# Kernel tuning notes

Hardware: AMD Instinct MI355X
Metric: run time of the kernel (lower is better)

Reference implementation:

```python
import jax, jax.numpy as jnp
import numpy as np

B, DIM, H, W = 32, 512, 48, 24


def conv1x1(x, w, b):
    # x: [B,C,H,W], w: [O,C], b: [O]  (torch Conv2d 1x1 weight squeezed)
    return jnp.einsum('bchw,oc->bohw', x, w) + b[None, :, None, None]


def setup_inputs() -> dict:
    key = jax.random.key(0)
    ks = jax.random.split(key, 14)
    s = 0.02
    inp = {
        'x': jax.random.normal(ks[0], (B, DIM, H, W), jnp.float32),
        'x_h': jax.random.normal(ks[1], (B, DIM, H, W), jnp.float32),
        'Wg': jax.random.normal(ks[2], (DIM, DIM), jnp.float32) * s,
        'bg': jax.random.normal(ks[3], (DIM,), jnp.float32) * s,
        'Wt': jax.random.normal(ks[4], (DIM, DIM), jnp.float32) * s,
        'bt': jax.random.normal(ks[5], (DIM,), jnp.float32) * s,
        'Wp': jax.random.normal(ks[6], (DIM, DIM), jnp.float32) * s,
        'bp': jax.random.normal(ks[7], (DIM,), jnp.float32) * s,
        'Ww': jax.random.normal(ks[8], (DIM, DIM), jnp.float32) * s,
        'bw': jax.random.normal(ks[9], (DIM,), jnp.float32) * s,
        'gamma': jax.random.normal(ks[10], (DIM,), jnp.float32) * 0.1,
        'beta': jax.random.normal(ks[11], (DIM,), jnp.float32) * 0.1,
        'run_mean': jax.random.normal(ks[12], (DIM,), jnp.float32) * 0.1,
        'run_var': jax.random.uniform(ks[13], (DIM,), jnp.float32, 0.5, 1.5),
    }
    return inp


def reference(x, x_h, Wg, bg, Wt, bt, Wp, bp, Ww, bw, gamma, beta, run_mean, run_var):
    Bsz, dim = x.shape[0], Wg.shape[0]
    g_x = conv1x1(x_h, Wg, bg).reshape(Bsz, dim, -1)      # [B,dim,N]
    theta_x = conv1x1(x, Wt, bt).reshape(Bsz, dim, -1)    # [B,dim,N]
    phi_x = conv1x1(x_h, Wp, bp).reshape(Bsz, dim, -1)    # [B,dim,N]
    # energy[b,i,j] = sum_n theta[b,i,n] * phi[b,j,n]  -> channel attention [B,dim,dim]
    energy = jnp.einsum('bin,bjn->bij', theta_x, phi_x)
    attention = energy / dim  # energy.size(-1) == dim
    y = jnp.einsum('bij,bjn->bin', attention, g_x).reshape(Bsz, dim, *x_h.shape[2:])
    W_y = conv1x1(y, Ww, bw)
    # BatchNorm2d in eval mode
    inv = gamma / jnp.sqrt(run_var + 1e-5)
    W_y = (W_y - run_mean[None, :, None, None]) * inv[None, :, None, None] + beta[None, :, None, None]
    return W_y + x
```

## Files before the change

kernel.cpp:

```cpp
#include <hip/hip_runtime.h>
#include <stdint.h>

typedef short short8 __attribute__((ext_vector_type(8)));
typedef float f32x4 __attribute__((ext_vector_type(4)));
typedef unsigned short u16;
typedef unsigned int u32;

struct alignas(8) U16x4 { u16 x, y, z, w; };

__device__ __forceinline__ u16 f2bf(float f) {
  u32 u = __float_as_uint(f);
  u += 0x7fffu + ((u >> 16) & 1u);
  return (u16)(u >> 16);
}
__device__ __forceinline__ float bf2f(u16 v) {
  return __uint_as_float(((u32)v) << 16);
}

__device__ __forceinline__ void gld_lds16(const u16* g, u16* l) {
  __builtin_amdgcn_global_load_lds((const __attribute__((address_space(1))) u32*)g,
                                   (__attribute__((address_space(3))) u32*)l,
                                   16, 0, 0);
}

__device__ __forceinline__ void mfma16x16x32(f32x4& c, short8 a, short8 b) {
  asm("v_mfma_f32_16x16x32_bf16 %0, %1, %2, %0" : "+v"(c) : "v"(a), "v"(b));
}

__device__ __forceinline__ float wave_red(float v) {
  for (int off = 32; off; off >>= 1) v += __shfl_down(v, off);
  return v;
}

template<int EPI>
__global__ void __launch_bounds__(512, 2) gemm_abt(
                         const u16* __restrict__ A, int64_t Abs,
                         const u16* __restrict__ Bt, int64_t Bbs,
                         void* __restrict__ Cptr, int64_t Cbs,
                         int M, int N, int K,
                         const float* __restrict__ v1,
                         const float* __restrict__ v2,
                         const float* __restrict__ v3,
                         const float* __restrict__ v4,
                         const u16* __restrict__ xres) {
  constexpr int BM = 256, BN = 128, BK = 32;
  extern __shared__ u16 lds[];
  u16* ldsA = lds;
  u16* ldsB = lds + 4 * (BM * BK);

  int bx, by, b;
  if (gridDim.z == 1) {
    const int nbx = N >> 7;
    const int bpb = nbx * (M >> 8);
    const int id = blockIdx.x;
    const int xcd = id & 7, rest = id >> 3;
    b = xcd + 8 * (rest / bpb);
    const int wi = rest % bpb;
    by = wi / nbx; bx = wi % nbx;
  } else {
    bx = blockIdx.x; by = blockIdx.y; b = blockIdx.z;
  }

  const u16* Ab = A + (int64_t)b * Abs;
  const u16* Bb = Bt + (int64_t)b * Bbs;
  const int brow = by * BM, bcol = bx * BN;
  const int tid = threadIdx.x, lane = tid & 63, w = tid >> 6;
  const int wr = w >> 1, wc = w & 1;

  f32x4 acc[4][4] = {};

  const int sr = tid >> 2;
  const int scs = ((tid & 3) ^ (sr & 3)) * 8;
  const int lo = sr * BK + (tid & 3) * 8;
  const u16* gA = Ab + (int64_t)(brow + sr) * K + scs;
  const u16* gB = Bb + (int64_t)(bcol + sr) * K + scs;

  const int la16 = lane & 15;
  const int kg = (lane >> 4) * 8;
  const int kc = kg ^ ((la16 & 3) * 8);
  const int nt = K / BK;

#define STAGE(buf, k0)                                              \
  do {                                                              \
    u16* la_ = ldsA + (buf) * (BM * BK) + lo;                       \
    u16* lb_ = ldsB + (buf) * (BN * BK) + lo;                       \
    gld_lds16(gA + (k0), la_);                                      \
    gld_lds16(gA + (int64_t)128 * K + (k0), la_ + 128 * BK);        \
    gld_lds16(gB + (k0), lb_);                                      \
  } while (0)

  STAGE(0, 0);
  STAGE(1, BK);
  STAGE(2, 2 * BK);

  for (int t = 0; t < nt; ++t) {
    __builtin_amdgcn_s_barrier();
    if (t + 3 < nt) {
      STAGE((t + 3) & 3, (t + 3) * BK);
      asm volatile("s_waitcnt vmcnt(9)" ::: "memory");
    } else {
      const int rem = nt - 1 - t;
      if (rem == 2)      asm volatile("s_waitcnt vmcnt(6)" ::: "memory");
      else if (rem == 1) asm volatile("s_waitcnt vmcnt(3)" ::: "memory");
      else               asm volatile("s_waitcnt vmcnt(0)" ::: "memory");
    }
    __builtin_amdgcn_s_barrier();
    __builtin_amdgcn_sched_barrier(0);
    const u16* as = ldsA + (t & 3) * (BM * BK);
    const u16* bs = ldsB + (t & 3) * (BN * BK);
    short8 af[4], bf[4];
#pragma unroll
    for (int m = 0; m < 4; ++m)
      af[m] = *(const short8*)&as[(wr * 64 + m * 16 + la16) * BK + kc];
#pragma unroll
    for (int n = 0; n < 4; ++n)
      bf[n] = *(const short8*)&bs[(wc * 64 + n * 16 + la16) * BK + kc];
    __builtin_amdgcn_s_setprio(1);
#pragma unroll
    for (int m = 0; m < 4; ++m)
#pragma unroll
      for (int n = 0; n < 4; ++n)
        mfma16x16x32(acc[m][n], af[m], bf[n]);
    __builtin_amdgcn_s_setprio(0);
  }
#undef STAGE
  asm volatile("s_nop 7\n\ts_nop 7");

  const int r0 = brow + wr * 64 + (lane >> 4) * 4;
  const int c0 = bcol + wc * 64 + la16;
  const int64_t b512 = (int64_t)b * 512;

  if (EPI == 4) {
    float* Cb = (float*)Cptr + (int64_t)b * Cbs;
    const u16* xb = xres + (int64_t)b * Cbs;
#pragma unroll
    for (int m = 0; m < 4; ++m) {
#pragma unroll
      for (int r = 0; r < 4; ++r) {
        const int row = r0 + m * 16 + r;
        const float scl = v1[row], shf = v2[b512 + row];
#pragma unroll
        for (int n = 0; n < 4; ++n) {
          const int col = c0 + n * 16;
          Cb[(int64_t)row * N + col] =
              acc[m][n][r] * scl + shf + bf2f(xb[(int64_t)row * N + col]);
        }
      }
    }
  } else {
    u16* Cb = (u16*)Cptr + (int64_t)b * Cbs;
#pragma unroll
    for (int m = 0; m < 4; ++m) {
#pragma unroll
      for (int r = 0; r < 4; ++r) {
        const int row = r0 + m * 16 + r;
        float a1 = 0.f, a3 = 0.f;
        if (EPI == 6) { a1 = v1[b512 + row]; a3 = v3[row]; }
#pragma unroll
        for (int n = 0; n < 4; ++n) {
          const int col = c0 + n * 16;
          float v = acc[m][n][r];
          if (EPI == 6) v += a1 * v2[col] + a3 * v4[b512 + col];
          Cb[(int64_t)row * N + col] = f2bf(v);
        }
      }
    }
  }
}

__global__ void prep_all(const float* __restrict__ x, const float* __restrict__ xh,
                         u16* __restrict__ xB, u16* __restrict__ xhB,
                         u16* __restrict__ xhT,
                         float* __restrict__ rx_part, float* __restrict__ rxh_part) {
  __shared__ float tl[64][65];
  __shared__ float rs[64];
  const int z = blockIdx.z;
  const int b = z & 31;
  const bool isxh = z >= 32;
  const float* src = (isxh ? xh : x) + (int64_t)b * 589824;
  u16* dstB = (isxh ? xhB : xB) + (int64_t)b * 589824;
  const int n0 = blockIdx.x * 64, c0 = blockIdx.y * 64;
  const int t = threadIdx.x;
  const int cl = t >> 4;
  const int q = t & 15;
#pragma unroll
  for (int p = 0; p < 4; ++p) {
    const int row = p * 16 + cl;
    const float4 v = *(const float4*)&src[(int64_t)(c0 + row) * 1152 + n0 + q * 4];
    tl[row][q * 4] = v.x; tl[row][q * 4 + 1] = v.y;
    tl[row][q * 4 + 2] = v.z; tl[row][q * 4 + 3] = v.w;
    U16x4 o = {f2bf(v.x), f2bf(v.y), f2bf(v.z), f2bf(v.w)};
    *(U16x4*)&dstB[(int64_t)(c0 + row) * 1152 + n0 + q * 4] = o;
    float pr = v.x + v.y + v.z + v.w;
    pr += __shfl_down(pr, 8); pr += __shfl_down(pr, 4);
    pr += __shfl_down(pr, 2); pr += __shfl_down(pr, 1);
    if (q == 0) rs[row] = pr;
  }
  __syncthreads();
  if (t < 64) {
    float* part = isxh ? rxh_part : rx_part;
    part[blockIdx.x * 16384 + b * 512 + c0 + t] = rs[t];
  }
  if (isxh) {
    const int n = t >> 2, cb = (t & 3) * 16;
    u16* dT = xhT + (int64_t)b * 589824 + (int64_t)(n0 + n) * 512 + c0 + cb;
#pragma unroll
    for (int j = 0; j < 4; ++j) {
      U16x4 o = {f2bf(tl[cb + 4 * j][n]), f2bf(tl[cb + 4 * j + 1][n]),
                 f2bf(tl[cb + 4 * j + 2][n]), f2bf(tl[cb + 4 * j + 3][n])};
      *(U16x4*)&dT[4 * j] = o;
    }
  }
}

__global__ void transpose_cvt4(const float* __restrict__ s0, const float* __restrict__ s1,
                               const float* __restrict__ s2, const float* __restrict__ s3,
                               u16* __restrict__ d0, u16* __restrict__ d1,
                               u16* __restrict__ d2, u16* __restrict__ d3) {
  const int z = blockIdx.z;
  const float* in = z == 0 ? s0 : z == 1 ? s1 : z == 2 ? s2 : s3;
  u16* out = z == 0 ? d0 : z == 1 ? d1 : z == 2 ? d2 : d3;
  __shared__ float t[32][33];
  const int n0 = blockIdx.x * 32, c0 = blockIdx.y * 32;
  const int tr = threadIdx.x >> 3, tc = (threadIdx.x & 7) * 4;
  const float4 v = *(const float4*)&in[(int64_t)(c0 + tr) * 512 + n0 + tc];
  t[tr][tc] = v.x; t[tr][tc + 1] = v.y; t[tr][tc + 2] = v.z; t[tr][tc + 3] = v.w;
  __syncthreads();
  U16x4 o;
  o.x = f2bf(t[tc][tr]); o.y = f2bf(t[tc + 1][tr]);
  o.z = f2bf(t[tc + 2][tr]); o.w = f2bf(t[tc + 3][tr]);
  *(U16x4*)&out[(int64_t)(n0 + tr) * 512 + c0 + tc] = o;
}

__global__ void cvt_kernel(const float* __restrict__ in, u16* __restrict__ out, int n4) {
  const int i = blockIdx.x * 256 + threadIdx.x;
  if (i < n4) {
    const float4 v = ((const float4*)in)[i];
    U16x4 o = {f2bf(v.x), f2bf(v.y), f2bf(v.z), f2bf(v.w)};
    ((U16x4*)out)[i] = o;
  }
}

__global__ void k_misc(const float* __restrict__ rx_part, const float* __restrict__ rxh_part,
                       float* __restrict__ rx, float* __restrict__ rxh,
                       const float* __restrict__ gamma, const float* __restrict__ beta,
                       const float* __restrict__ mean, const float* __restrict__ var,
                       const float* __restrict__ bw,
                       const float* __restrict__ bp, const float* __restrict__ bg,
                       float* __restrict__ sc2, float* __restrict__ shift0,
                       float* __restrict__ s2) {
  if (blockIdx.x < 64) {
    const int i = blockIdx.x * 256 + threadIdx.x;
    float s = 0;
#pragma unroll 3
    for (int p = 0; p < 18; ++p) s += rxh_part[p * 16384 + i];
    rxh[i] = s;
  } else if (blockIdx.x < 128) {
    const int i = (blockIdx.x - 64) * 256 + threadIdx.x;
    float s = 0;
#pragma unroll 3
    for (int p = 0; p < 18; ++p) s += rx_part[p * 16384 + i];
    rx[i] = s;
  } else {
    for (int c = threadIdx.x; c < 512; c += 256) {
      const float sc = gamma[c] * rsqrtf(var[c] + 1e-5f);
      sc2[c] = sc * (1.0f / 512.0f);
      shift0[c] = (bw[c] - mean[c]) * sc + beta[c];
    }
    if (threadIdx.x < 64) {
      float p = 0;
      for (int k = threadIdx.x; k < 512; k += 64) p += bp[k] * bg[k];
      p = wave_red(p);
      if (threadIdx.x == 0) s2[0] = p;
    }
  }
}

__global__ void k_mv1(const float* __restrict__ Wp, const float* __restrict__ Wt,
                      const float* __restrict__ Ww,
                      const u16* __restrict__ WpT, const u16* __restrict__ WgT,
                      const float* __restrict__ bg, const float* __restrict__ bt,
                      const float* __restrict__ bp,
                      const float* __restrict__ rx, const float* __restrict__ rxh,
                      float* __restrict__ sigphi, float* __restrict__ tau2,
                      float* __restrict__ h1, float* __restrict__ w1,
                      float* __restrict__ c2) {
  const int wid = blockIdx.x * 4 + (threadIdx.x >> 6);
  const int lane = threadIdx.x & 63;
  float dot = 0;
  if (wid < 16384) {
    const int b = wid >> 9, t = wid & 511;
    const float* wr = Wp + (int64_t)t * 512;
    const float* vr = rxh + b * 512;
#pragma unroll
    for (int k = 0; k < 8; ++k) dot += wr[lane + k * 64] * vr[lane + k * 64];
    dot = wave_red(dot);
    if (lane == 0) sigphi[wid] = dot;
  } else if (wid < 32768) {
    const int r = wid - 16384, b = r >> 9, t = r & 511;
    const float* wr = Wt + (int64_t)t * 512;
    const float* vr = rx + b * 512;
#pragma unroll
    for (int k = 0; k < 8; ++k) dot += wr[lane + k * 64] * vr[lane + k * 64];
    dot = wave_red(dot);
    if (lane == 0) tau2[r] = dot + 1152.0f * bt[t];
  } else if (wid < 33280) {
    const int j = wid - 32768;
    const u16* wr = WpT + (int64_t)j * 512;
#pragma unroll
    for (int k = 0; k < 8; ++k) dot += bf2f(wr[lane + k * 64]) * bg[lane + k * 64];
    dot = wave_red(dot);
    if (lane == 0) h1[j] = dot;
  } else if (wid < 33792) {
    const int c = wid - 33280;
    const float* wr = Ww + (int64_t)c * 512;
#pragma unroll
    for (int k = 0; k < 8; ++k) dot += wr[lane + k * 64] * bt[lane + k * 64];
    dot = wave_red(dot);
    if (lane == 0) w1[c] = dot;
  } else {
    const int e = wid - 33792;
    const u16* wr = WgT + (int64_t)e * 512;
#pragma unroll
    for (int k = 0; k < 8; ++k) dot += bf2f(wr[lane + k * 64]) * bp[lane + k * 64];
    dot = wave_red(dot);
    if (lane == 0) c2[e] = dot;
  }
}

__global__ void k_mv2(const u16* __restrict__ WgT, const float* __restrict__ Ww,
                      const float* __restrict__ bg,
                      const float* __restrict__ sigphi, const float* __restrict__ tau2,
                      float* __restrict__ c1, float* __restrict__ w2,
                      float* __restrict__ s1) {
  const int wid = blockIdx.x * 4 + (threadIdx.x >> 6);
  const int lane = threadIdx.x & 63;
  float dot = 0;
  if (wid < 16384) {
    const int b = wid >> 9, t = wid & 511;
    const u16* wr = WgT + (int64_t)t * 512;
    const float* vr = sigphi + b * 512;
#pragma unroll
    for (int k = 0; k < 8; ++k) dot += bf2f(wr[lane + k * 64]) * vr[lane + k * 64];
    dot = wave_red(dot);
    if (lane == 0) c1[wid] = dot;
  } else if (wid < 32768) {
    const int r = wid - 16384, b = r >> 9, t = r & 511;
    const float* wr = Ww + (int64_t)t * 512;
    const float* vr = tau2 + b * 512;
#pragma unroll
    for (int k = 0; k < 8; ++k) dot += wr[lane + k * 64] * vr[lane + k * 64];
    dot = wave_red(dot);
    if (lane == 0) w2[r] = dot;
  } else if (wid < 32800) {
    const int b = wid - 32768;
    const float* vr = sigphi + b * 512;
#pragma unroll
    for (int k = 0; k < 8; ++k) dot += vr[lane + k * 64] * bg[lane + k * 64];
    dot = wave_red(dot);
    if (lane == 0) s1[b] = dot;
  }
}

__global__ void k_shiftv(const u16* __restrict__ R, const float* __restrict__ h1,
                         const float* __restrict__ w1, const float* __restrict__ w2,
                         const float* __restrict__ s1, const float* __restrict__ s2,
                         const float* __restrict__ sc2, const float* __restrict__ shift0,
                         float* __restrict__ shiftv) {
  const int wid = blockIdx.x * 4 + (threadIdx.x >> 6);
  const int lane = threadIdx.x & 63;
  const int b = wid >> 9, c = wid & 511;
  const u16* rr = R + (int64_t)b * 262144 + (int64_t)c * 512;
  float dot = 0;
#pragma unroll
  for (int k = 0; k < 8; ++k) dot += bf2f(rr[lane + k * 64]) * h1[lane + k * 64];
  dot = wave_red(dot);
  if (lane == 0)
    shiftv[wid] = sc2[c] * (dot + s1[b] * w1[c] + s2[0] * w2[wid]) + shift0[c];
}

extern "C" void kernel_launch(void* const* d_in, const int* in_sizes, int n_in,
                              void* d_out, int out_size, void* d_ws, size_t ws_size,
                              hipStream_t stream) {
  const float* x     = (const float*)d_in[0];
  const float* x_h   = (const float*)d_in[1];
  const float* Wg    = (const float*)d_in[2];
  const float* bg    = (const float*)d_in[3];
  const float* Wt    = (const float*)d_in[4];
  const float* bt    = (const float*)d_in[5];
  const float* Wp    = (const float*)d_in[6];
  const float* bp    = (const float*)d_in[7];
  const float* Ww    = (const float*)d_in[8];
  const float* bw    = (const float*)d_in[9];
  const float* gamma = (const float*)d_in[10];
  const float* beta  = (const float*)d_in[11];
  const float* rmean = (const float*)d_in[12];
  const float* rvar  = (const float*)d_in[13];
  float* out = (float*)d_out;

  const int Bsz = 32, D = 512, N = 1152;
  const int64_t DN = (int64_t)D * N;
  const int64_t DD = (int64_t)D * D;
  const size_t LDSB = 98304;

  char* ws = (char*)d_ws;
  const size_t KB = 1024, MB = 1048576;
  u16* WtT  = (u16*)(ws + 0);
  u16* WpT  = (u16*)(ws + 512 * KB);
  u16* WwB  = (u16*)(ws + 1 * MB);
  u16* WgT  = (u16*)(ws + 1 * MB + 512 * KB);
  u16* WaB  = (u16*)(ws + 2 * MB);
  u16* WbTB = (u16*)(ws + 2 * MB + 512 * KB);
  float* rx     = (float*)(ws + 3 * MB + 512 * KB);
  float* rxh    = (float*)(ws + 3 * MB + 576 * KB);
  float* sigphi = (float*)(ws + 3 * MB + 640 * KB);
  float* tau2   = (float*)(ws + 3 * MB + 704 * KB);
  float* c1     = (float*)(ws + 3 * MB + 768 * KB);
  float* w2     = (float*)(ws + 3 * MB + 832 * KB);
  float* shiftv = (float*)(ws + 3 * MB + 896 * KB);
  float* h1     = (float*)(ws + 3 * MB + 960 * KB);
  float* w1     = (float*)(ws + 3 * MB + 962 * KB);
  float* c2     = (float*)(ws + 3 * MB + 964 * KB);
  float* sc2    = (float*)(ws + 3 * MB + 968 * KB);
  float* shift0 = (float*)(ws + 3 * MB + 970 * KB);
  float* s1     = (float*)(ws + 3 * MB + 972 * KB);
  float* s2     = (float*)(ws + 3 * MB + 974 * KB);
  u16* xB  = (u16*)(ws + 4 * MB);
  u16* xhB = (u16*)(ws + 40 * MB);
  u16* xhT = (u16*)(ws + 76 * MB);
  u16* SD1 = (u16*)(ws + 112 * MB);
  u16* SD2 = (u16*)(ws + 130 * MB);
  float* rx_part  = (float*)(ws + 148 * MB);
  float* rxh_part = (float*)(ws + 150 * MB);

  prep_all<<<dim3(18, 8, 64), 256, 0, stream>>>(x, x_h, xB, xhB, xhT,
                                                rx_part, rxh_part);
  transpose_cvt4<<<dim3(16, 16, 4), 256, 0, stream>>>(Wt, Wp, Wg, Ww, WtT, WpT, WgT,
                                                      (u16*)(ws + 152 * MB) );
  cvt_kernel<<<dim3(D * D / 4 / 256), 256, 0, stream>>>(Ww, WwB, D * D / 4);
  k_misc<<<dim3(129), 256, 0, stream>>>(rx_part, rxh_part, rx, rxh, gamma, beta,
                                        rmean, rvar, bw, bp, bg, sc2, shift0, s2);
  k_mv1<<<dim3(8576), 256, 0, stream>>>(Wp, Wt, Ww, WpT, WgT, bg, bt, bp, rx, rxh,
                                        sigphi, tau2, h1, w1, c2);
  k_mv2<<<dim3(8200), 256, 0, stream>>>(WgT, Ww, bg, sigphi, tau2, c1, w2, s1);
  gemm_abt<0><<<dim3(4, 2, 2), 512, LDSB, stream>>>(
      WwB, DD, WtT, DD, WaB, DD, D, D, D, nullptr, nullptr, nullptr, nullptr, nullptr);

  gemm_abt<0><<<dim3(8 * Bsz), 512, LDSB, stream>>>(
      xhB, DN, xB, DN, SD1, DD, D, D, N, nullptr, nullptr, nullptr, nullptr, nullptr);
  gemm_abt<0><<<dim3(8 * Bsz), 512, LDSB, stream>>>(
      WaB, 0, SD1, DD, SD2, DD, D, D, D, nullptr, nullptr, nullptr, nullptr, nullptr);
  k_shiftv<<<dim3(4096), 256, 0, stream>>>(SD2, h1, w1, w2, s1, s2, sc2, shift0, shiftv);
  gemm_abt<6><<<dim3(8 * Bsz), 512, LDSB, stream>>>(
      SD2, DD, WbTB, 0, SD1, DD, D, D, D, w2, c2, w1, c1, nullptr);
  gemm_abt<4><<<dim3(18 * Bsz), 512, LDSB, stream>>>(
      SD1, DD, xhT, DN, out, DN, D, N, D, sc2, shiftv, nullptr, nullptr, xB);
}
```

Measured before the change: 208.2 us.

## Split input prep into row-wise convert/sum and a register bf16 transpose

Replaces the fused tile kernel, which converted x/x_h to bf16, wrote partial row sums and transposed x_h through LDS, with a per-row kernel that converts and fully reduces each channel row directly. A separate kernel then transposes the bf16 x_h in registers using 8x8 short8 blocks. This removes the partial-sum buffers and their reduction pass in k_misc, and drops the unused fourth weight transpose. The cost is an extra read of xhB (bf16) and one more launch, plus very small 256-thread blocks per row that leave threads idle.

```diff
diff --git a/kernel.cpp b/kernel.cpp
--- a/kernel.cpp
+++ b/kernel.cpp
@@ -168,48 +168,46 @@
   }
 }
 
-__global__ void prep_all(const float* __restrict__ x, const float* __restrict__ xh,
+__global__ void cvt_row2(const float* __restrict__ x, const float* __restrict__ xh,
                          u16* __restrict__ xB, u16* __restrict__ xhB,
-                         u16* __restrict__ xhT,
-                         float* __restrict__ rx_part, float* __restrict__ rxh_part) {
-  __shared__ float tl[64][65];
-  __shared__ float rs[64];
-  const int z = blockIdx.z;
-  const int b = z & 31;
-  const bool isxh = z >= 32;
-  const float* src = (isxh ? xh : x) + (int64_t)b * 589824;
-  u16* dstB = (isxh ? xhB : xB) + (int64_t)b * 589824;
-  const int n0 = blockIdx.x * 64, c0 = blockIdx.y * 64;
+                         float* __restrict__ rx, float* __restrict__ rxh) {
+  const int64_t row = blockIdx.x;
+  const float* in = blockIdx.y ? xh : x;
+  u16* out = blockIdx.y ? xhB : xB;
+  float* rs = blockIdx.y ? rxh : rx;
+  const float4* ib = (const float4*)(in + row * 1152);
+  U16x4* ob = (U16x4*)(out + row * 1152);
+  float s = 0.f;
+  for (int i = threadIdx.x; i < 288; i += 256) {
+    float4 v = ib[i];
+    s += v.x + v.y + v.z + v.w;
+    U16x4 o = {f2bf(v.x), f2bf(v.y), f2bf(v.z), f2bf(v.w)};
+    ob[i] = o;
+  }
+  s = wave_red(s);
+  __shared__ float red[4];
+  if ((threadIdx.x & 63) == 0) red[threadIdx.x >> 6] = s;
+  __syncthreads();
+  if (threadIdx.x == 0) rs[row] = red[0] + red[1] + red[2] + red[3];
+}
+
+__global__ void transpose_bf_reg(const u16* __restrict__ in, u16* __restrict__ out) {
+  const int b = blockIdx.z;
+  const u16* ib = in + (int64_t)b * 589824;
+  u16* ob = out + (int64_t)b * 589824;
   const int t = threadIdx.x;
-  const int cl = t >> 4;
-  const int q = t & 15;
-#pragma unroll
-  for (int p = 0; p < 4; ++p) {
-    const int row = p * 16 + cl;
-    const float4 v = *(const float4*)&src[(int64_t)(c0 + row) * 1152 + n0 + q * 4];
-    tl[row][q * 4] = v.x; tl[row][q * 4 + 1] = v.y;
-    tl[row][q * 4 + 2] = v.z; tl[row][q * 4 + 3] = v.w;
-    U16x4 o = {f2bf(v.x), f2bf(v.y), f2bf(v.z), f2bf(v.w)};
-    *(U16x4*)&dstB[(int64_t)(c0 + row) * 1152 + n0 + q * 4] = o;
-    float pr = v.x + v.y + v.z + v.w;
-    pr += __shfl_down(pr, 8); pr += __shfl_down(pr, 4);
-    pr += __shfl_down(pr, 2); pr += __shfl_down(pr, 1);
-    if (q == 0) rs[row] = pr;
-  }
-  __syncthreads();
-  if (t < 64) {
-    float* part = isxh ? rxh_part : rx_part;
-    part[blockIdx.x * 16384 + b * 512 + c0 + t] = rs[t];
-  }
-  if (isxh) {
-    const int n = t >> 2, cb = (t & 3) * 16;
-    u16* dT = xhT + (int64_t)b * 589824 + (int64_t)(n0 + n) * 512 + c0 + cb;
-#pragma unroll
-    for (int j = 0; j < 4; ++j) {
-      U16x4 o = {f2bf(tl[cb + 4 * j][n]), f2bf(tl[cb + 4 * j + 1][n]),
-                 f2bf(tl[cb + 4 * j + 2][n]), f2bf(tl[cb + 4 * j + 3][n])};
-      *(U16x4*)&dT[4 * j] = o;
-    }
+  const int c0 = blockIdx.y * 128 + (t & 15) * 8;
+  const int n0 = blockIdx.x * 128 + (t >> 4) * 8;
+  short8 r[8];
+#pragma unroll
+  for (int k = 0; k < 8; ++k)
+    r[k] = *(const short8*)&ib[(int64_t)(c0 + k) * 1152 + n0];
+#pragma unroll
+  for (int i = 0; i < 8; ++i) {
+    short8 wv;
+#pragma unroll
+    for (int k = 0; k < 8; ++k) wv[k] = r[k][i];
+    *(short8*)&ob[(int64_t)(n0 + i) * 512 + c0] = wv;
   }
 }
 
@@ -241,38 +239,21 @@
   }
 }
 
-__global__ void k_misc(const float* __restrict__ rx_part, const float* __restrict__ rxh_part,
-                       float* __restrict__ rx, float* __restrict__ rxh,
-                       const float* __restrict__ gamma, const float* __restrict__ beta,
-                       const float* __restrict__ mean, const float* __restrict__ var,
-                       const float* __restrict__ bw,
-                       const float* __restrict__ bp, const float* __restrict__ bg,
-                       float* __restrict__ sc2, float* __restrict__ shift0,
-                       float* __restrict__ s2) {
-  if (blockIdx.x < 64) {
-    const int i = blockIdx.x * 256 + threadIdx.x;
-    float s = 0;
-#pragma unroll 3
-    for (int p = 0; p < 18; ++p) s += rxh_part[p * 16384 + i];
-    rxh[i] = s;
-  } else if (blockIdx.x < 128) {
-    const int i = (blockIdx.x - 64) * 256 + threadIdx.x;
-    float s = 0;
-#pragma unroll 3
-    for (int p = 0; p < 18; ++p) s += rx_part[p * 16384 + i];
-    rx[i] = s;
-  } else {
-    for (int c = threadIdx.x; c < 512; c += 256) {
-      const float sc = gamma[c] * rsqrtf(var[c] + 1e-5f);
-      sc2[c] = sc * (1.0f / 512.0f);
-      shift0[c] = (bw[c] - mean[c]) * sc + beta[c];
-    }
-    if (threadIdx.x < 64) {
-      float p = 0;
-      for (int k = threadIdx.x; k < 512; k += 64) p += bp[k] * bg[k];
-      p = wave_red(p);
-      if (threadIdx.x == 0) s2[0] = p;
-    }
+__global__ void k_small(const float* __restrict__ gamma, const float* __restrict__ beta,
+                        const float* __restrict__ mean, const float* __restrict__ var,
+                        const float* __restrict__ bw,
+                        const float* __restrict__ bp, const float* __restrict__ bg,
+                        float* __restrict__ sc2, float* __restrict__ shift0,
+                        float* __restrict__ s2) {
+  const int c = threadIdx.x;
+  const float sc = gamma[c] * rsqrtf(var[c] + 1e-5f);
+  sc2[c] = sc * (1.0f / 512.0f);
+  shift0[c] = (bw[c] - mean[c]) * sc + beta[c];
+  if (c < 64) {
+    float p = 0;
+    for (int k = c; k < 512; k += 64) p += bp[k] * bg[k];
+    p = wave_red(p);
+    if (c == 0) s2[0] = p;
   }
 }
 
@@ -430,16 +411,14 @@
   u16* xhT = (u16*)(ws + 76 * MB);
   u16* SD1 = (u16*)(ws + 112 * MB);
   u16* SD2 = (u16*)(ws + 130 * MB);
-  float* rx_part  = (float*)(ws + 148 * MB);
-  float* rxh_part = (float*)(ws + 150 * MB);
-
-  prep_all<<<dim3(18, 8, 64), 256, 0, stream>>>(x, x_h, xB, xhB, xhT,
-                                                rx_part, rxh_part);
-  transpose_cvt4<<<dim3(16, 16, 4), 256, 0, stream>>>(Wt, Wp, Wg, Ww, WtT, WpT, WgT,
-                                                      (u16*)(ws + 152 * MB) );
+
+  cvt_row2<<<dim3(Bsz * D, 2), 256, 0, stream>>>(x, x_h, xB, xhB, rx, rxh);
+  transpose_bf_reg<<<dim3(9, 4, Bsz), 256, 0, stream>>>(xhB, xhT);
+  transpose_cvt4<<<dim3(16, 16, 3), 256, 0, stream>>>(Wt, Wp, Wg, nullptr,
+                                                      WtT, WpT, WgT, nullptr);
   cvt_kernel<<<dim3(D * D / 4 / 256), 256, 0, stream>>>(Ww, WwB, D * D / 4);
-  k_misc<<<dim3(129), 256, 0, stream>>>(rx_part, rxh_part, rx, rxh, gamma, beta,
-                                        rmean, rvar, bw, bp, bg, sc2, shift0, s2);
+  k_small<<<dim3(1), 512, 0, stream>>>(gamma, beta, rmean, rvar, bw, bp, bg,
+                                       sc2, shift0, s2);
   k_mv1<<<dim3(8576), 256, 0, stream>>>(Wp, Wt, Ww, WpT, WgT, bg, bt, bp, rx, rxh,
                                         sigphi, tau2, h1, w1, c2);
   k_mv2<<<dim3(8200), 256, 0, stream>>>(WgT, Ww, bg, sigphi, tau2, c1, w2, s1);
```

New measurement: 212.3 us. About the same (+2.0%).
